# Kernel optimization log

Measured on AMD Instinct MI355X. Metric: run time of the kernel, lower is better.

The kernel has to match this reference:

```python
import jax, jax.numpy as jnp
import numpy as np

L, H, E, HS, T, B, V, BS = 12, 12, 768, 64, 1024, 4, 50257, 1024
EPS = 1e-8
SCALE = E ** -0.5  # NOTE: original code scales by n_embd**-0.5, not head_size**-0.5


def _ln(x, g, b):
    mu = jnp.mean(x, axis=-1, keepdims=True)
    var = jnp.mean((x - mu) ** 2, axis=-1, keepdims=True)
    return (x - mu) / jnp.sqrt(var + EPS) * g + b


def setup_inputs() -> dict:
    key = jax.random.key(0)
    ks = iter(jax.random.split(key, 32))
    s = 0.02
    inp = {
        "idx": jax.random.randint(next(ks), (B, T), 0, V, dtype=jnp.int64),
        "tok_emb": jax.random.normal(next(ks), (V, E), jnp.float32) * s,
        "pos_emb": jax.random.normal(next(ks), (BS, E), jnp.float32) * s,
        "wq": jax.random.normal(next(ks), (L, H, E, HS), jnp.float32) * s,
        "wk": jax.random.normal(next(ks), (L, H, E, HS), jnp.float32) * s,
        "wv": jax.random.normal(next(ks), (L, H, E, HS), jnp.float32) * s,
        "proj_w": jax.random.normal(next(ks), (L, E, E), jnp.float32) * s,
        "proj_b": jnp.zeros((L, E), jnp.float32),
        "ln1_g": jnp.ones((L, E), jnp.float32),
        "ln1_b": jnp.zeros((L, E), jnp.float32),
        "ln2_g": jnp.ones((L, E), jnp.float32),
        "ln2_b": jnp.zeros((L, E), jnp.float32),
        "w1": jax.random.normal(next(ks), (L, E, 4 * E), jnp.float32) * s,
        "b1": jnp.zeros((L, 4 * E), jnp.float32),
        "w2": jax.random.normal(next(ks), (L, 4 * E, E), jnp.float32) * s,
        "b2": jnp.zeros((L, E), jnp.float32),
        "lnf_g": jnp.ones((E,), jnp.float32),
        "lnf_b": jnp.zeros((E,), jnp.float32),
        "head_w": jax.random.normal(next(ks), (E, V), jnp.float32) * s,
        "head_b": jnp.zeros((V,), jnp.float32),
    }
    return inp


def reference(idx, tok_emb, pos_emb, wq, wk, wv, proj_w, proj_b,
              ln1_g, ln1_b, ln2_g, ln2_b, w1, b1, w2, b2,
              lnf_g, lnf_b, head_w, head_b):
    x = tok_emb[idx] + pos_emb[jnp.arange(T)][None, :, :]  # [B,T,E]
    mask = jnp.tril(jnp.ones((T, T), bool))
    neg = jnp.finfo(x.dtype).min
    for l in range(L):
        # --- multi-head attention ---
        xn = _ln(x, ln1_g[l], ln1_b[l])
        q = jnp.einsum("bte,hed->bhtd", xn, wq[l])
        k = jnp.einsum("bte,hed->bhtd", xn, wk[l])
        v = jnp.einsum("bte,hed->bhtd", xn, wv[l])
        scores = jnp.einsum("bhtd,bhsd->bhts", q, k) * SCALE
        scores = jnp.where(mask, scores, neg)
        attn = jax.nn.softmax(scores, axis=-1)
        o = jnp.einsum("bhts,bhsd->bhtd", attn, v)  # [B,H,T,HS]
        o = o.transpose(0, 2, 1, 3).reshape(B, T, E)
        x = x + o @ proj_w[l].T + proj_b[l]
        # --- feed-forward ---
        xn = _ln(x, ln2_g[l], ln2_b[l])
        h = jax.nn.gelu(xn @ w1[l] + b1[l], approximate=False)
        x = x + h @ w2[l] + b2[l]
    x = _ln(x, lnf_g, lnf_b)
    logits = x @ head_w + head_b  # [B,T,V]
    return logits
```

## Files before the change

### kernel.cpp

```cpp
#include <hip/hip_runtime.h>
#include <hip/hip_bf16.h>
#include <stdint.h>
#include <math.h>

typedef __hip_bfloat16 bf16;
typedef short s16x8 __attribute__((ext_vector_type(8)));
typedef short s16x4 __attribute__((ext_vector_type(4)));
typedef float f32x4 __attribute__((ext_vector_type(4)));

#define SCALE_QK 0.03608439182435161f
#define NEG_BIG  -1.0e30f

__device__ __forceinline__ void lds_dma16(void* lds_uniform, const void* gsrc) {
  __builtin_amdgcn_global_load_lds(
      (const __attribute__((address_space(1))) unsigned int*)(uintptr_t)gsrc,
      (__attribute__((address_space(3))) unsigned int*)(unsigned int)(uintptr_t)lds_uniform,
      16, 0, 0);
}

enum { EPI_BF16 = 0, EPI_GELU = 1, EPI_RES = 2, EPI_HEAD = 3 };

template <int EPI>
__global__ __launch_bounds__(256)
void gemm_bt(const bf16* __restrict__ A, const bf16* __restrict__ BT,
             const float* __restrict__ bias, float* Cf, bf16* Cb,
             int M, int N, int K, int Nreal)
{
  __shared__ __align__(16) bf16 As[2][128 * 32];
  __shared__ __align__(16) bf16 Bs[2][128 * 32];
  const int tid = threadIdx.x;
  const int w = tid >> 6, l = tid & 63;
  const int lo = l & 15, hi = l >> 4;
  const int wm = (w & 1) * 64, wn = (w >> 1) * 64;
  const long row0 = (long)blockIdx.y * 128;
  const long col0 = (long)blockIdx.x * 128;

  const int c0 = w * 64 + l, c1 = c0 + 256;
  const bf16* a0 = A + (row0 + (c0 >> 2)) * K + (c0 & 3) * 8;
  const bf16* a1 = A + (row0 + (c1 >> 2)) * K + (c1 & 3) * 8;
  const bf16* b0 = BT + (col0 + (c0 >> 2)) * K + (c0 & 3) * 8;
  const bf16* b1 = BT + (col0 + (c1 >> 2)) * K + (c1 & 3) * 8;
  const int w512 = w * 512;

  const f32x4 zero4 = {0.f, 0.f, 0.f, 0.f};
  f32x4 acc[4][4];
#pragma unroll
  for (int m = 0; m < 4; ++m)
#pragma unroll
    for (int n = 0; n < 4; ++n) acc[m][n] = zero4;

  const int nk = K >> 5;
  lds_dma16(&As[0][w512],        a0);
  lds_dma16(&As[0][2048 + w512], a1);
  lds_dma16(&Bs[0][w512],        b0);
  lds_dma16(&Bs[0][2048 + w512], b1);
  __syncthreads();

  int cur = 0;
  for (int t = 0; t < nk; ++t) {
    if (t + 1 < nk) {
      const int kt = (t + 1) << 5;
      lds_dma16(&As[cur ^ 1][w512],        a0 + kt);
      lds_dma16(&As[cur ^ 1][2048 + w512], a1 + kt);
      lds_dma16(&Bs[cur ^ 1][w512],        b0 + kt);
      lds_dma16(&Bs[cur ^ 1][2048 + w512], b1 + kt);
    }
    s16x8 af[4], bfr[4];
#pragma unroll
    for (int m = 0; m < 4; ++m)
      af[m] = *(const s16x8*)&As[cur][(wm + m * 16 + lo) * 32 + hi * 8];
#pragma unroll
    for (int n = 0; n < 4; ++n)
      bfr[n] = *(const s16x8*)&Bs[cur][(wn + n * 16 + lo) * 32 + hi * 8];
#pragma unroll
    for (int m = 0; m < 4; ++m)
#pragma unroll
      for (int n = 0; n < 4; ++n)
        acc[m][n] = __builtin_amdgcn_mfma_f32_16x16x32_bf16(af[m], bfr[n], acc[m][n], 0, 0, 0);
    __syncthreads();
    cur ^= 1;
  }

#pragma unroll
  for (int m = 0; m < 4; ++m) {
#pragma unroll
    for (int n = 0; n < 4; ++n) {
      const long col = col0 + wn + n * 16 + lo;
#pragma unroll
      for (int r = 0; r < 4; ++r) {
        const long row = row0 + wm + m * 16 + hi * 4 + r;
        float v = acc[m][n][r];
        if constexpr (EPI == EPI_BF16) {
          Cb[row * N + col] = __float2bfloat16(v);
        } else if constexpr (EPI == EPI_GELU) {
          v += bias[col];
          v = 0.5f * v * (1.f + erff(v * 0.70710678118654752f));
          Cb[row * N + col] = __float2bfloat16(v);
        } else if constexpr (EPI == EPI_RES) {
          Cf[row * N + col] += v + bias[col];
        } else {
          if (col < Nreal) Cf[row * Nreal + col] = v + bias[col];
        }
      }
    }
  }
}

__global__ __launch_bounds__(256)
void attn_kernel(const bf16* __restrict__ qkv, bf16* __restrict__ o)
{
  __shared__ __align__(16) bf16 Kl[64 * 64];
  __shared__ __align__(16) bf16 Vl[64 * 64];
  __shared__ __align__(16) bf16 Pl[4][32 * 64];
  const int tid = threadIdx.x;
  const int w = tid >> 6, l = tid & 63;
  const int lo = l & 15, hi = l >> 4;
  const int q0 = blockIdx.x * 128;
  const int b = blockIdx.y / 12, h = blockIdx.y % 12;
  const int wq0 = q0 + w * 32;
  const bf16* base = qkv + (long)b * 1024 * 2304;

  s16x8 qf[2][2];
#pragma unroll
  for (int m = 0; m < 2; ++m)
#pragma unroll
    for (int ks = 0; ks < 2; ++ks)
      qf[m][ks] = *(const s16x8*)(base + (long)(wq0 + m * 16 + lo) * 2304 + h * 64 + ks * 32 + hi * 8);

  const f32x4 zero4 = {0.f, 0.f, 0.f, 0.f};
  f32x4 oacc[2][4];
  float mst[2][4], lst[2][4];
#pragma unroll
  for (int m = 0; m < 2; ++m) {
#pragma unroll
    for (int n = 0; n < 4; ++n) oacc[m][n] = zero4;
#pragma unroll
    for (int r = 0; r < 4; ++r) { mst[m][r] = -3.0e38f; lst[m][r] = 0.f; }
  }

  const int cB = tid + 256;

  const int nt = (q0 + 128) / 64;
  for (int t = 0; t < nt; ++t) {
    const int j0 = t * 64;
    const s16x8 rk0 = *(const s16x8*)(base + (long)(j0 + (tid >> 3)) * 2304 +  768 + h * 64 + (tid & 7) * 8);
    const s16x8 rk1 = *(const s16x8*)(base + (long)(j0 + (cB  >> 3)) * 2304 +  768 + h * 64 + (cB  & 7) * 8);
    const s16x8 rv0 = *(const s16x8*)(base + (long)(j0 + (tid >> 3)) * 2304 + 1536 + h * 64 + (tid & 7) * 8);
    const s16x8 rv1 = *(const s16x8*)(base + (long)(j0 + (cB  >> 3)) * 2304 + 1536 + h * 64 + (cB  & 7) * 8);
    __syncthreads();
    *(s16x8*)&Kl[tid * 8] = rk0;
    *(s16x8*)&Kl[cB  * 8] = rk1;
    *(s16x8*)&Vl[tid * 8] = rv0;
    *(s16x8*)&Vl[cB  * 8] = rv1;
    __syncthreads();

    if (j0 <= wq0 + 31) {
      f32x4 s[2][4];
#pragma unroll
      for (int m = 0; m < 2; ++m)
#pragma unroll
        for (int n = 0; n < 4; ++n) s[m][n] = zero4;
#pragma unroll
      for (int ks = 0; ks < 2; ++ks) {
        s16x8 kf[4];
#pragma unroll
        for (int n = 0; n < 4; ++n)
          kf[n] = *(const s16x8*)&Kl[(n * 16 + lo) * 64 + ks * 32 + hi * 8];
#pragma unroll
        for (int m = 0; m < 2; ++m)
#pragma unroll
          for (int n = 0; n < 4; ++n)
            s[m][n] = __builtin_amdgcn_mfma_f32_16x16x32_bf16(qf[m][ks], kf[n], s[m][n], 0, 0, 0);
      }
      const bool edge = (j0 + 63 > wq0);
#pragma unroll
      for (int m = 0; m < 2; ++m)
#pragma unroll
        for (int n = 0; n < 4; ++n) {
          const int j = j0 + n * 16 + lo;
#pragma unroll
          for (int r = 0; r < 4; ++r) {
            float v = s[m][n][r] * SCALE_QK;
            if (edge && j > wq0 + m * 16 + hi * 4 + r) v = NEG_BIG;
            s[m][n][r] = v;
          }
        }
#pragma unroll
      for (int m = 0; m < 2; ++m)
#pragma unroll
        for (int r = 0; r < 4; ++r) {
          float x = fmaxf(fmaxf(s[m][0][r], s[m][1][r]), fmaxf(s[m][2][r], s[m][3][r]));
          x = fmaxf(x, __shfl_xor(x, 1));
          x = fmaxf(x, __shfl_xor(x, 2));
          x = fmaxf(x, __shfl_xor(x, 4));
          x = fmaxf(x, __shfl_xor(x, 8));
          const float mn = fmaxf(mst[m][r], x);
          const float corr = __expf(mst[m][r] - mn);
          mst[m][r] = mn;
          float rs = 0.f;
#pragma unroll
          for (int n = 0; n < 4; ++n) {
            float p = __expf(s[m][n][r] - mn);
            s[m][n][r] = p;
            rs += p;
          }
          rs += __shfl_xor(rs, 1);
          rs += __shfl_xor(rs, 2);
          rs += __shfl_xor(rs, 4);
          rs += __shfl_xor(rs, 8);
          lst[m][r] = lst[m][r] * corr + rs;
#pragma unroll
          for (int n = 0; n < 4; ++n) oacc[m][n][r] *= corr;
        }
#pragma unroll
      for (int m = 0; m < 2; ++m)
#pragma unroll
        for (int n = 0; n < 4; ++n)
#pragma unroll
          for (int r = 0; r < 4; ++r)
            Pl[w][(m * 16 + hi * 4 + r) * 64 + n * 16 + lo] = __float2bfloat16(s[m][n][r]);
      s16x8 pa[2][2];
#pragma unroll
      for (int m = 0; m < 2; ++m)
#pragma unroll
        for (int ks = 0; ks < 2; ++ks)
          pa[m][ks] = *(const s16x8*)&Pl[w][(m * 16 + lo) * 64 + ks * 32 + hi * 8];
#pragma unroll
      for (int ks = 0; ks < 2; ++ks)
#pragma unroll
        for (int n = 0; n < 4; ++n) {
          s16x8 vf;
#pragma unroll
          for (int j = 0; j < 8; ++j)
            vf[j] = *(const short*)&Vl[(ks * 32 + hi * 8 + j) * 64 + n * 16 + lo];
#pragma unroll
          for (int m = 0; m < 2; ++m)
            oacc[m][n] = __builtin_amdgcn_mfma_f32_16x16x32_bf16(pa[m][ks], vf, oacc[m][n], 0, 0, 0);
        }
    }
  }
#pragma unroll
  for (int m = 0; m < 2; ++m)
#pragma unroll
    for (int n = 0; n < 4; ++n)
#pragma unroll
      for (int r = 0; r < 4; ++r) {
        const int q = wq0 + m * 16 + hi * 4 + r;
        o[(long)(b * 1024 + q) * 768 + h * 64 + n * 16 + lo] =
            __float2bfloat16(oacc[m][n][r] / lst[m][r]);
      }
}

__global__ void detect_idx(const int* __restrict__ idx, int* __restrict__ flag)
{
  const int t = threadIdx.x;
  const int v = idx[2 * t + 1];
  const unsigned long long nz = __ballot(v != 0);
  if (t == 0) flag[0] = (nz == 0ull) ? 1 : 0;
}

__global__ __launch_bounds__(192)
void embed_kernel(const int* __restrict__ idx, const float* __restrict__ tok,
                  const float* __restrict__ pos, float* __restrict__ x,
                  const int* __restrict__ flag)
{
  const int row = blockIdx.x;
  const int t = row & 1023;
  const int id = flag[0] ? idx[2 * row] : idx[row];
  const int e = threadIdx.x * 4;
  const float4 a = *(const float4*)&tok[(long)id * 768 + e];
  const float4 p = *(const float4*)&pos[(long)t * 768 + e];
  float4 r; r.x = a.x + p.x; r.y = a.y + p.y; r.z = a.z + p.z; r.w = a.w + p.w;
  *(float4*)&x[(long)row * 768 + e] = r;
}

__global__ __launch_bounds__(256)
void ln_kernel(const float* __restrict__ x, const float* __restrict__ g,
               const float* __restrict__ bt, bf16* __restrict__ out)
{
  const int row = blockIdx.x, tid = threadIdx.x;
  const float* xr = x + (long)row * 768;
  const float v0 = xr[tid], v1 = xr[tid + 256], v2 = xr[tid + 512];
  float s = v0 + v1 + v2;
  float q = v0 * v0 + v1 * v1 + v2 * v2;
#pragma unroll
  for (int o = 32; o > 0; o >>= 1) { s += __shfl_down(s, o); q += __shfl_down(q, o); }
  __shared__ float sh[8];
  const int w = tid >> 6;
  if ((tid & 63) == 0) { sh[w] = s; sh[4 + w] = q; }
  __syncthreads();
  s = sh[0] + sh[1] + sh[2] + sh[3];
  q = sh[4] + sh[5] + sh[6] + sh[7];
  const float mu = s * (1.f / 768.f);
  const float var = q * (1.f / 768.f) - mu * mu;
  const float rs = rsqrtf(var + 1e-8f);
  bf16* orow = out + (long)row * 768;
  orow[tid]       = __float2bfloat16((v0 - mu) * rs * g[tid] + bt[tid]);
  orow[tid + 256] = __float2bfloat16((v1 - mu) * rs * g[tid + 256] + bt[tid + 256]);
  orow[tid + 512] = __float2bfloat16((v2 - mu) * rs * g[tid + 512] + bt[tid + 512]);
}

__device__ __forceinline__ void tile_tr64(const float* __restrict__ ip,
                                          bf16* __restrict__ op,
                                          int R, int Creal, int r0, int c0,
                                          int tid, float (*tile)[65])
{
  const int tx = tid & 63, ty = tid >> 6;
#pragma unroll
  for (int p = 0; p < 16; ++p) {
    const int r = p * 4 + ty;
    const int c = c0 + tx;
    tile[r][tx] = (c < Creal) ? ip[(long)(r0 + r) * Creal + c] : 0.f;
  }
  __syncthreads();
#pragma unroll
  for (int p = 0; p < 16; ++p) {
    const int cc = p * 4 + ty;
    op[(long)(c0 + cc) * R + r0 + tx] = __float2bfloat16(tile[tx][cc]);
  }
}

__global__ __launch_bounds__(256)
void transpose_conv(const float* __restrict__ in, bf16* __restrict__ out,
                    int R, int Creal)
{
  __shared__ float tile[64][65];
  tile_tr64(in, out, R, Creal, blockIdx.y * 64, blockIdx.x * 64, threadIdx.x, tile);
}

__global__ __launch_bounds__(256)
void repack_layer(const float* __restrict__ wq, const float* __restrict__ wk,
                  const float* __restrict__ wv, const float* __restrict__ projw,
                  const float* __restrict__ w1, const float* __restrict__ w2,
                  bf16* __restrict__ WqkvT, bf16* __restrict__ WprojT,
                  bf16* __restrict__ W1T, bf16* __restrict__ W2T)
{
  __shared__ float tile[64][65];
  const int tid = threadIdx.x;
  const int t = blockIdx.x;
  if (t < 432) {
    const int op_i = t / 144, r = t % 144;
    const int h = r / 12, ry = r % 12;
    const float* ip = (op_i == 0 ? wq : op_i == 1 ? wk : wv) + h * 49152;
    bf16* op = WqkvT + (long)op_i * 768 * 768 + (long)h * 64 * 768;
    tile_tr64(ip, op, 768, 64, ry * 64, 0, tid, tile);
  } else if (t < 576) {
    const int t2 = t - 432;
    const int r0 = (t2 / 12) * 64, c0 = (t2 % 12) * 64;
#pragma unroll
    for (int p = 0; p < 4; ++p) {
      const int row = r0 + p * 16 + (tid >> 4);
      const int col = c0 + (tid & 15) * 4;
      const float4 v = *(const float4*)&projw[(long)row * 768 + col];
      bf16 t0 = __float2bfloat16(v.x), t1 = __float2bfloat16(v.y);
      bf16 t2b = __float2bfloat16(v.z), t3 = __float2bfloat16(v.w);
      s16x4 pk;
      pk[0] = *(const short*)&t0; pk[1] = *(const short*)&t1;
      pk[2] = *(const short*)&t2b; pk[3] = *(const short*)&t3;
      *(s16x4*)&WprojT[(long)row * 768 + col] = pk;
    }
  } else if (t < 1152) {
    const int t3 = t - 576;
    tile_tr64(w1, W1T, 768, 3072, (t3 / 48) * 64, (t3 % 48) * 64, tid, tile);
  } else {
    const int t4 = t - 1152;
    tile_tr64(w2, W2T, 3072, 768, (t4 / 12) * 64, (t4 % 12) * 64, tid, tile);
  }
}

extern "C" void kernel_launch(void* const* d_in, const int* in_sizes, int n_in,
                              void* d_out, int out_size, void* d_ws, size_t ws_size,
                              hipStream_t stream)
{
  (void)in_sizes; (void)n_in; (void)out_size; (void)ws_size;
  const int*   idx   = (const int*)d_in[0];
  const float* tok   = (const float*)d_in[1];
  const float* pos   = (const float*)d_in[2];
  const float* wq    = (const float*)d_in[3];
  const float* wk    = (const float*)d_in[4];
  const float* wv    = (const float*)d_in[5];
  const float* projw = (const float*)d_in[6];
  const float* projb = (const float*)d_in[7];
  const float* ln1g  = (const float*)d_in[8];
  const float* ln1b  = (const float*)d_in[9];
  const float* ln2g  = (const float*)d_in[10];
  const float* ln2b  = (const float*)d_in[11];
  const float* w1    = (const float*)d_in[12];
  const float* b1    = (const float*)d_in[13];
  const float* w2    = (const float*)d_in[14];
  const float* b2    = (const float*)d_in[15];
  const float* lnfg  = (const float*)d_in[16];
  const float* lnfb  = (const float*)d_in[17];
  const float* headw = (const float*)d_in[18];
  const float* headb = (const float*)d_in[19];
  float* out = (float*)d_out;

  char* ws = (char*)d_ws;
  size_t off = 0;
  auto alloc = [&](size_t bytes) -> void* {
    void* p = ws + off; off += (bytes + 255) & ~(size_t)255; return p;
  };
  int*   iflag  = (int*)  alloc(256);
  float* x      = (float*)alloc(4096ull * 768 * 4);
  bf16*  xn     = (bf16*) alloc(4096ull * 768 * 2);
  bf16*  qkvb   = (bf16*) alloc(4096ull * 2304 * 2);
  bf16*  ob     = (bf16*) alloc(4096ull * 768 * 2);
  bf16*  hb     = (bf16*) alloc(4096ull * 3072 * 2);
  bf16*  WqkvT  = (bf16*) alloc(2304ull * 768 * 2);
  bf16*  WprojT = (bf16*) alloc(768ull * 768 * 2);
  bf16*  W1T    = (bf16*) alloc(3072ull * 768 * 2);
  bf16*  W2T    = (bf16*) alloc(768ull * 3072 * 2);
  bf16*  headT  = (bf16*) alloc(50304ull * 768 * 2);

  detect_idx<<<1, 64, 0, stream>>>(idx, iflag);
  transpose_conv<<<dim3(786, 12), 256, 0, stream>>>(headw, headT, 768, 50257);
  embed_kernel<<<4096, 192, 0, stream>>>(idx, tok, pos, x, iflag);

  for (int l = 0; l < 12; ++l) {
    const size_t hOff = (size_t)l * 12 * 768 * 64;
    repack_layer<<<1728, 256, 0, stream>>>(wq + hOff, wk + hOff, wv + hOff,
                                           projw + (size_t)l * 768 * 768,
                                           w1 + (size_t)l * 768 * 3072,
                                           w2 + (size_t)l * 3072 * 768,
                                           WqkvT, WprojT, W1T, W2T);

    ln_kernel<<<4096, 256, 0, stream>>>(x, ln1g + l * 768, ln1b + l * 768, xn);
    gemm_bt<EPI_BF16><<<dim3(18, 32), 256, 0, stream>>>(xn, WqkvT, nullptr, nullptr, qkvb, 4096, 2304, 768, 2304);
    attn_kernel<<<dim3(8, 48), 256, 0, stream>>>(qkvb, ob);
    gemm_bt<EPI_RES><<<dim3(6, 32), 256, 0, stream>>>(ob, WprojT, projb + l * 768, x, nullptr, 4096, 768, 768, 768);
    ln_kernel<<<4096, 256, 0, stream>>>(x, ln2g + l * 768, ln2b + l * 768, xn);
    gemm_bt<EPI_GELU><<<dim3(24, 32), 256, 0, stream>>>(xn, W1T, b1 + (size_t)l * 3072, nullptr, hb, 4096, 3072, 768, 3072);
    gemm_bt<EPI_RES><<<dim3(6, 32), 256, 0, stream>>>(hb, W2T, b2 + l * 768, x, nullptr, 4096, 768, 3072, 768);
  }

  ln_kernel<<<4096, 256, 0, stream>>>(x, lnfg, lnfb, xn);
  gemm_bt<EPI_HEAD><<<dim3(393, 32), 256, 0, stream>>>(xn, headT, headb, out, nullptr, 4096, 50304, 768, 50257);
}
```

Before: 3.742 ms.

## Use 256x128 tile head GEMM and one-wavefront-per-row vectorized layernorm

Adds a dedicated LM-head GEMM kernel with 512 threads and a 256x128 output tile, which halves A/B tile reloads per output compared with the generic 128-row kernel. It double-buffers LDS through direct global-to-LDS loads. Layernorm is rewritten so each wavefront handles one row with float4 loads, xor-shuffle reduction and packed bf16 stores. This removes the shared-memory reduction and the block barrier. The larger tile uses more LDS and registers per block, which may reduce occupancy.

```diff
diff --git a/kernel.cpp b/kernel.cpp
--- a/kernel.cpp
+++ b/kernel.cpp
@@ -106,6 +106,77 @@
   }
 }
 
+__global__ __launch_bounds__(512)
+void gemm_head256(const bf16* __restrict__ A, const bf16* __restrict__ BT,
+                  const float* __restrict__ bias, float* __restrict__ Cf,
+                  int K, int Nreal)
+{
+  __shared__ __align__(16) bf16 As[2][256 * 32];
+  __shared__ __align__(16) bf16 Bs[2][128 * 32];
+  const int tid = threadIdx.x;
+  const int w = tid >> 6, l = tid & 63;
+  const int lo = l & 15, hi = l >> 4;
+  const int wm = (w & 3) * 64, wn = (w >> 2) * 64;
+  const long row0 = (long)blockIdx.y * 256;
+  const long col0 = (long)blockIdx.x * 128;
+
+  const bf16* a0 = A + (row0 + (tid >> 2)) * K + (tid & 3) * 8;
+  const bf16* a1 = A + (row0 + 128 + (tid >> 2)) * K + (tid & 3) * 8;
+  const bf16* b0 = BT + (col0 + (tid >> 2)) * K + (tid & 3) * 8;
+  const int w512 = w * 512;
+
+  const f32x4 zero4 = {0.f, 0.f, 0.f, 0.f};
+  f32x4 acc[4][4];
+#pragma unroll
+  for (int m = 0; m < 4; ++m)
+#pragma unroll
+    for (int n = 0; n < 4; ++n) acc[m][n] = zero4;
+
+  const int nk = K >> 5;
+  lds_dma16(&As[0][w512],        a0);
+  lds_dma16(&As[0][4096 + w512], a1);
+  lds_dma16(&Bs[0][w512],        b0);
+  __syncthreads();
+
+  int cur = 0;
+  for (int t = 0; t < nk; ++t) {
+    if (t + 1 < nk) {
+      const int kt = (t + 1) << 5;
+      lds_dma16(&As[cur ^ 1][w512],        a0 + kt);
+      lds_dma16(&As[cur ^ 1][4096 + w512], a1 + kt);
+      lds_dma16(&Bs[cur ^ 1][w512],        b0 + kt);
+    }
+    s16x8 af[4], bfr[4];
+#pragma unroll
+    for (int m = 0; m < 4; ++m)
+      af[m] = *(const s16x8*)&As[cur][(wm + m * 16 + lo) * 32 + hi * 8];
+#pragma unroll
+    for (int n = 0; n < 4; ++n)
+      bfr[n] = *(const s16x8*)&Bs[cur][(wn + n * 16 + lo) * 32 + hi * 8];
+#pragma unroll
+    for (int m = 0; m < 4; ++m)
+#pragma unroll
+      for (int n = 0; n < 4; ++n)
+        acc[m][n] = __builtin_amdgcn_mfma_f32_16x16x32_bf16(af[m], bfr[n], acc[m][n], 0, 0, 0);
+    __syncthreads();
+    cur ^= 1;
+  }
+
+#pragma unroll
+  for (int m = 0; m < 4; ++m) {
+#pragma unroll
+    for (int n = 0; n < 4; ++n) {
+      const long col = col0 + wn + n * 16 + lo;
+#pragma unroll
+      for (int r = 0; r < 4; ++r) {
+        const long row = row0 + wm + m * 16 + hi * 4 + r;
+        if (col < Nreal)
+          Cf[row * Nreal + col] = acc[m][n][r] + bias[col];
+      }
+    }
+  }
+}
+
 __global__ __launch_bounds__(256)
 void attn_kernel(const bf16* __restrict__ qkv, bf16* __restrict__ o)
 {
@@ -278,26 +349,34 @@
 void ln_kernel(const float* __restrict__ x, const float* __restrict__ g,
                const float* __restrict__ bt, bf16* __restrict__ out)
 {
-  const int row = blockIdx.x, tid = threadIdx.x;
+  const int lane = threadIdx.x & 63;
+  const int row = blockIdx.x * 4 + (threadIdx.x >> 6);
   const float* xr = x + (long)row * 768;
-  const float v0 = xr[tid], v1 = xr[tid + 256], v2 = xr[tid + 512];
-  float s = v0 + v1 + v2;
-  float q = v0 * v0 + v1 * v1 + v2 * v2;
-#pragma unroll
-  for (int o = 32; o > 0; o >>= 1) { s += __shfl_down(s, o); q += __shfl_down(q, o); }
-  __shared__ float sh[8];
-  const int w = tid >> 6;
-  if ((tid & 63) == 0) { sh[w] = s; sh[4 + w] = q; }
-  __syncthreads();
-  s = sh[0] + sh[1] + sh[2] + sh[3];
-  q = sh[4] + sh[5] + sh[6] + sh[7];
+  f32x4 v[3];
+  float s = 0.f, q = 0.f;
+#pragma unroll
+  for (int p = 0; p < 3; ++p) {
+    v[p] = *(const f32x4*)&xr[lane * 4 + p * 256];
+#pragma unroll
+    for (int j = 0; j < 4; ++j) { s += v[p][j]; q += v[p][j] * v[p][j]; }
+  }
+#pragma unroll
+  for (int o = 32; o > 0; o >>= 1) { s += __shfl_xor(s, o); q += __shfl_xor(q, o); }
   const float mu = s * (1.f / 768.f);
   const float var = q * (1.f / 768.f) - mu * mu;
   const float rs = rsqrtf(var + 1e-8f);
   bf16* orow = out + (long)row * 768;
-  orow[tid]       = __float2bfloat16((v0 - mu) * rs * g[tid] + bt[tid]);
-  orow[tid + 256] = __float2bfloat16((v1 - mu) * rs * g[tid + 256] + bt[tid + 256]);
-  orow[tid + 512] = __float2bfloat16((v2 - mu) * rs * g[tid + 512] + bt[tid + 512]);
+#pragma unroll
+  for (int p = 0; p < 3; ++p) {
+    const int e = lane * 4 + p * 256;
+    s16x4 pk;
+#pragma unroll
+    for (int j = 0; j < 4; ++j) {
+      bf16 t = __float2bfloat16((v[p][j] - mu) * rs * g[e + j] + bt[e + j]);
+      pk[j] = *(const short*)&t;
+    }
+    *(s16x4*)&orow[e] = pk;
+  }
 }
 
 __device__ __forceinline__ void tile_tr64(const float* __restrict__ ip,
@@ -424,15 +503,15 @@
                                            w2 + (size_t)l * 3072 * 768,
                                            WqkvT, WprojT, W1T, W2T);
 
-    ln_kernel<<<4096, 256, 0, stream>>>(x, ln1g + l * 768, ln1b + l * 768, xn);
+    ln_kernel<<<1024, 256, 0, stream>>>(x, ln1g + l * 768, ln1b + l * 768, xn);
     gemm_bt<EPI_BF16><<<dim3(18, 32), 256, 0, stream>>>(xn, WqkvT, nullptr, nullptr, qkvb, 4096, 2304, 768, 2304);
     attn_kernel<<<dim3(8, 48), 256, 0, stream>>>(qkvb, ob);
     gemm_bt<EPI_RES><<<dim3(6, 32), 256, 0, stream>>>(ob, WprojT, projb + l * 768, x, nullptr, 4096, 768, 768, 768);
-    ln_kernel<<<4096, 256, 0, stream>>>(x, ln2g + l * 768, ln2b + l * 768, xn);
+    ln_kernel<<<1024, 256, 0, stream>>>(x, ln2g + l * 768, ln2b + l * 768, xn);
     gemm_bt<EPI_GELU><<<dim3(24, 32), 256, 0, stream>>>(xn, W1T, b1 + (size_t)l * 3072, nullptr, hb, 4096, 3072, 768, 3072);
     gemm_bt<EPI_RES><<<dim3(6, 32), 256, 0, stream>>>(hb, W2T, b2 + l * 768, x, nullptr, 4096, 768, 3072, 768);
   }
 
-  ln_kernel<<<4096, 256, 0, stream>>>(x, lnfg, lnfb, xn);
-  gemm_bt<EPI_HEAD><<<dim3(393, 32), 256, 0, stream>>>(xn, headT, headb, out, nullptr, 4096, 50304, 768, 50257);
-}
+  ln_kernel<<<1024, 256, 0, stream>>>(x, lnfg, lnfb, xn);
+  gemm_head256<<<dim3(393, 16), 512, 0, stream>>>(xn, headT, headb, out, 768, 50257);
+}
```

After: 3.625 ms. 1.03x faster.
